# Performance work log

Hardware: AMD Instinct MI355X
Metric: run time of the kernel (lower is better)

The kernel has to match this reference:

```python
import jax, jax.numpy as jnp
import numpy as np

HISTORY = 128  # self-inclusive causal window width

def _layernorm(x, g, b, eps=1e-5):
    mu = jnp.mean(x, axis=-1, keepdims=True)
    var = jnp.var(x, axis=-1, keepdims=True)
    return (x - mu) * jax.lax.rsqrt(var + eps) * g + b

def setup_inputs() -> dict:
    key = jax.random.key(0)
    ks = jax.random.split(key, 8)
    dim, hid, B, T = 64, 256, 4, 4096
    s = lambda fan_in: 1.0 / np.sqrt(fan_in)
    return {
        "x": jax.random.normal(ks[0], (B, T, dim), jnp.float32),
        "W_in": jax.random.normal(ks[1], (dim, hid), jnp.float32) * s(dim),
        "b_in": jnp.zeros((hid,), jnp.float32),
        "W_qkv": jax.random.normal(ks[2], (hid, 3 * hid), jnp.float32) * s(hid),
        "b_qkv": jnp.zeros((3 * hid,), jnp.float32),
        "g_attn": jnp.ones((hid,), jnp.float32),
        "be_attn": jnp.zeros((hid,), jnp.float32),
        "g_mlp": jnp.ones((hid,), jnp.float32),
        "be_mlp": jnp.zeros((hid,), jnp.float32),
        "W1": jax.random.normal(ks[3], (hid, hid), jnp.float32) * s(hid),
        "b1": jnp.zeros((hid,), jnp.float32),
        "W2": jax.random.normal(ks[4], (hid, hid), jnp.float32) * s(hid),
        "b2": jnp.zeros((hid,), jnp.float32),
        "W_out": jax.random.normal(ks[5], (hid, dim), jnp.float32) * s(hid),
        "b_out": jnp.zeros((dim,), jnp.float32),
    }

def reference(x, W_in, b_in, W_qkv, b_qkv, g_attn, be_attn, g_mlp, be_mlp,
              W1, b1, W2, b2, W_out, b_out):
    B, T, _ = x.shape
    hid = W_in.shape[1]
    h = x @ W_in + b_in                                  # (B,T,hid)
    qkv = _layernorm(h, g_attn, be_attn) @ W_qkv + b_qkv
    q, k, v = jnp.split(qkv, 3, axis=-1)
    scale = 1.0 / jnp.sqrt(jnp.asarray(hid, x.dtype))
    scores = jnp.einsum('bqd,bkd->bqk', q, k) * scale    # (B,T,T)
    idx = jnp.arange(T)
    delta = idx[:, None] - idx[None, :]
    mask = (delta >= 0) & (delta <= HISTORY)             # self-inclusive window
    scores = jnp.where(mask[None], scores, jnp.finfo(x.dtype).min)
    attn = jax.nn.softmax(scores, axis=-1)
    attn_out = jnp.einsum('bqk,bkd->bqd', attn, v)
    h = h + attn_out                                     # residual (dropout=0)
    m = _layernorm(h, g_mlp, be_mlp)
    m = jax.nn.gelu(m @ W1 + b1, approximate=False) @ W2 + b2
    h = h + m
    return h @ W_out + b_out                             # (B,T,dim)
```

## Files before the change

kernel.cpp:

```cpp
#include <hip/hip_runtime.h>
#include <hip/hip_bf16.h>
#include <math.h>

typedef short bf8 __attribute__((ext_vector_type(8)));
typedef float f4  __attribute__((ext_vector_type(4)));

#define DEV static __device__ __forceinline__

DEV f4 MFMA(bf8 a, bf8 b, f4 c) { return __builtin_amdgcn_mfma_f32_16x16x32_bf16(a, b, c, 0, 0, 0); }

DEV unsigned short f2bf(float f) {
  union { float f; unsigned int u; } v; v.f = f;
  unsigned int r = v.u + 0x7FFFu + ((v.u >> 16) & 1u);
  return (unsigned short)(r >> 16);
}
DEV float bf2f(unsigned short u) {
  union { unsigned int u; float f; } v; v.u = ((unsigned int)u) << 16;
  return v.f;
}

struct P15 { const void* p[15]; };

DEV float ldin(const void* p, int i, bool bf) {
  return bf ? bf2f(((const unsigned short*)p)[i]) : ((const float*)p)[i];
}

#define PB_IN 0
#define PB_QKV 256
#define PB1 1024
#define PB2 1280
#define PB_OUT 1536
#define PGA 1600
#define PBA 1856
#define PGM 2112
#define PBM 2368

__global__ __launch_bounds__(256) void k_prep(P15 in,
    unsigned short* __restrict__ xb, unsigned short* __restrict__ WinT,
    unsigned short* __restrict__ WqkvT, unsigned short* __restrict__ W1T,
    unsigned short* __restrict__ W2T, unsigned short* __restrict__ WoutT,
    float* __restrict__ par)
{
  const bool bf = (*(const unsigned int*)in.p[5]) == 0x3F803F80u;
  const int E0 = 1048576;
  const int E1 = E0 + 16384;
  const int E2 = E1 + 196608;
  const int E3 = E2 + 65536;
  const int E4 = E3 + 65536;
  const int E5 = E4 + 16384;
  const int E6 = E5 + 2624;
  for (int i = blockIdx.x * 256 + threadIdx.x; i < E6; i += gridDim.x * 256) {
    if (i < E0) {
      xb[i] = f2bf(ldin(in.p[0], i, bf));
    } else if (i < E1) {
      int j = i - E0, n = j >> 6, k = j & 63;
      WinT[j] = f2bf(ldin(in.p[1], k * 256 + n, bf));
    } else if (i < E2) {
      int j = i - E1, n = j >> 8, k = j & 255;
      WqkvT[j] = f2bf(ldin(in.p[3], k * 768 + n, bf));
    } else if (i < E3) {
      int j = i - E2, n = j >> 8, k = j & 255;
      W1T[j] = f2bf(ldin(in.p[9], k * 256 + n, bf));
    } else if (i < E4) {
      int j = i - E3, n = j >> 8, k = j & 255;
      W2T[j] = f2bf(ldin(in.p[11], k * 256 + n, bf));
    } else if (i < E5) {
      int j = i - E4, n = j >> 8, k = j & 255;
      WoutT[j] = f2bf(ldin(in.p[13], k * 64 + n, bf));
    } else {
      int j = i - E5;
      const void* src; int o;
      if (j < 256)       { src = in.p[2];  o = j; }
      else if (j < 1024) { src = in.p[4];  o = j - 256; }
      else if (j < 1280) { src = in.p[10]; o = j - 1024; }
      else if (j < 1536) { src = in.p[12]; o = j - 1280; }
      else if (j < 1600) { src = in.p[14]; o = j - 1536; }
      else if (j < 1856) { src = in.p[5];  o = j - 1600; }
      else if (j < 2112) { src = in.p[6];  o = j - 1856; }
      else if (j < 2368) { src = in.p[7];  o = j - 2112; }
      else               { src = in.p[8];  o = j - 2368; }
      par[j] = ldin(src, o, bf);
    }
  }
}

__global__ __launch_bounds__(256) void k_in_ln(const unsigned short* __restrict__ xb,
    const unsigned short* __restrict__ WinT, const float* __restrict__ par,
    float* __restrict__ h, unsigned short* __restrict__ ln1)
{
  __shared__ unsigned short sA[64 * 72];
  __shared__ unsigned short sB[256 * 72];
  const int tid = threadIdx.x, lane = tid & 63, w = tid >> 6;
  const int l15 = lane & 15, l4 = lane >> 4;
  const int m0 = blockIdx.x * 64;
  for (int t = tid; t < 512; t += 256) {
    int r = t >> 3, c8 = (t & 7) * 8;
    *(bf8*)&sA[r * 72 + c8] = *(const bf8*)&xb[(m0 + r) * 64 + c8];
  }
  for (int t = tid; t < 2048; t += 256) {
    int r = t >> 3, c8 = (t & 7) * 8;
    *(bf8*)&sB[r * 72 + c8] = *(const bf8*)&WinT[r * 64 + c8];
  }
  __syncthreads();
  f4 z = {0.f, 0.f, 0.f, 0.f};
  f4 acc[16];
  #pragma unroll
  for (int f = 0; f < 16; ++f) acc[f] = z;
  #pragma unroll
  for (int ks = 0; ks < 2; ++ks) {
    bf8 a = *(const bf8*)&sA[(16 * w + l15) * 72 + ks * 32 + l4 * 8];
    #pragma unroll
    for (int f = 0; f < 16; ++f) {
      bf8 b = *(const bf8*)&sB[(16 * f + l15) * 72 + ks * 32 + l4 * 8];
      acc[f] = MFMA(a, b, acc[f]);
    }
  }
  float s[4] = {0,0,0,0}, s2[4] = {0,0,0,0};
  #pragma unroll
  for (int f = 0; f < 16; ++f) {
    float bias = par[PB_IN + 16 * f + l15];
    #pragma unroll
    for (int r = 0; r < 4; ++r) {
      float v = acc[f][r] + bias; acc[f][r] = v;
      s[r] += v; s2[r] += v * v;
    }
  }
  #pragma unroll
  for (int msk = 1; msk <= 8; msk <<= 1) {
    #pragma unroll
    for (int r = 0; r < 4; ++r) { s[r] += __shfl_xor(s[r], msk); s2[r] += __shfl_xor(s2[r], msk); }
  }
  float mu[4], rstd[4];
  #pragma unroll
  for (int r = 0; r < 4; ++r) {
    mu[r] = s[r] * (1.f / 256.f);
    float var = s2[r] * (1.f / 256.f) - mu[r] * mu[r];
    rstd[r] = rsqrtf(var + 1e-5f);
  }
  #pragma unroll
  for (int f = 0; f < 16; ++f) {
    int col = 16 * f + l15;
    float g = par[PGA + col], be = par[PBA + col];
    #pragma unroll
    for (int r = 0; r < 4; ++r) {
      int row = m0 + 16 * w + 4 * l4 + r;
      h[row * 256 + col] = acc[f][r];
      ln1[row * 256 + col] = f2bf((acc[f][r] - mu[r]) * rstd[r] * g + be);
    }
  }
}

__global__ __launch_bounds__(256) void k_qkv(const unsigned short* __restrict__ ln1,
    const unsigned short* __restrict__ WqkvT, const float* __restrict__ par,
    unsigned short* __restrict__ qb, unsigned short* __restrict__ kb,
    unsigned short* __restrict__ vT)
{
  __shared__ unsigned short sA[64 * 72];
  __shared__ unsigned short sB[64 * 72];
  const int tid = threadIdx.x, lane = tid & 63, w = tid >> 6;
  const int l15 = lane & 15, l4 = lane >> 4;
  const int mt = blockIdx.x / 12, nt = blockIdx.x % 12;
  const int m0 = mt * 64, n0 = nt * 64;
  const int wm = w >> 1, wn = w & 1;
  f4 z = {0.f, 0.f, 0.f, 0.f};
  f4 acc[2][2];
  acc[0][0] = z; acc[0][1] = z; acc[1][0] = z; acc[1][1] = z;
  for (int kc = 0; kc < 4; ++kc) {
    for (int t = tid; t < 512; t += 256) {
      int r = t >> 3, c8 = (t & 7) * 8;
      *(bf8*)&sA[r * 72 + c8] = *(const bf8*)&ln1[(m0 + r) * 256 + kc * 64 + c8];
    }
    for (int t = tid; t < 512; t += 256) {
      int r = t >> 3, c8 = (t & 7) * 8;
      *(bf8*)&sB[r * 72 + c8] = *(const bf8*)&WqkvT[(n0 + r) * 256 + kc * 64 + c8];
    }
    __syncthreads();
    #pragma unroll
    for (int ks = 0; ks < 2; ++ks) {
      bf8 a0 = *(const bf8*)&sA[(32 * wm + l15) * 72 + ks * 32 + l4 * 8];
      bf8 a1 = *(const bf8*)&sA[(32 * wm + 16 + l15) * 72 + ks * 32 + l4 * 8];
      bf8 b0 = *(const bf8*)&sB[(32 * wn + l15) * 72 + ks * 32 + l4 * 8];
      bf8 b1 = *(const bf8*)&sB[(32 * wn + 16 + l15) * 72 + ks * 32 + l4 * 8];
      acc[0][0] = MFMA(a0, b0, acc[0][0]);
      acc[0][1] = MFMA(a0, b1, acc[0][1]);
      acc[1][0] = MFMA(a1, b0, acc[1][0]);
      acc[1][1] = MFMA(a1, b1, acc[1][1]);
    }
    __syncthreads();
  }
  #pragma unroll
  for (int i = 0; i < 2; ++i) {
    #pragma unroll
    for (int j = 0; j < 2; ++j) {
      int col = n0 + 32 * wn + 16 * j + l15;
      float bias = par[PB_QKV + col];
      int seg = col >> 8, c = col & 255;
      #pragma unroll
      for (int r = 0; r < 4; ++r) {
        int row = m0 + 32 * wm + 16 * i + 4 * l4 + r;
        unsigned short ov = f2bf(acc[i][j][r] + bias);
        if (seg == 0) qb[row * 256 + c] = ov;
        else if (seg == 1) kb[row * 256 + c] = ov;
        else vT[((row >> 12) * 256 + c) * 4096 + (row & 4095)] = ov;
      }
    }
  }
}

__global__ __launch_bounds__(256) void k_attn(const unsigned short* __restrict__ qb,
    const unsigned short* __restrict__ kb, const unsigned short* __restrict__ vT,
    const float* __restrict__ h, const float* __restrict__ par,
    float* __restrict__ h2, unsigned short* __restrict__ ln2)
{
  __shared__ unsigned short sKV[256 * 72];
  __shared__ unsigned short sP[64 * 200];
  const int tid = threadIdx.x, lane = tid & 63, w = tid >> 6;
  const int l15 = lane & 15, l4 = lane >> 4;
  const int b = blockIdx.x >> 6, q0 = (blockIdx.x & 63) * 64;
  const int tok0 = b * 4096 + q0, kstart = q0 - 128;

  bf8 qreg[8];
  {
    const int qrow = tok0 + 16 * w + l15;
    #pragma unroll
    for (int ks = 0; ks < 8; ++ks)
      qreg[ks] = *(const bf8*)&qb[qrow * 256 + ks * 32 + l4 * 8];
  }

  f4 z = {0.f, 0.f, 0.f, 0.f};
  f4 sacc[12];
  #pragma unroll
  for (int i = 0; i < 12; ++i) sacc[i] = z;

  #pragma unroll
  for (int c = 0; c < 3; ++c) {
    for (int t = tid; t < 2048; t += 256) {
      int r = t >> 5, c8 = (t & 31) * 8;
      int j = kstart + 64 * c + r; if (j < 0) j = 0;
      *(bf8*)&sKV[r * 264 + c8] = *(const bf8*)&kb[(b * 4096 + j) * 256 + c8];
    }
    __syncthreads();
    #pragma unroll
    for (int ks = 0; ks < 8; ++ks) {
      #pragma unroll
      for (int fn = 0; fn < 4; ++fn) {
        bf8 bfr = *(const bf8*)&sKV[(16 * fn + l15) * 264 + ks * 32 + l4 * 8];
        sacc[4 * c + fn] = MFMA(qreg[ks], bfr, sacc[4 * c + fn]);
      }
    }
    __syncthreads();
  }

  const float scale = 0.0625f;
  float mx[4] = {-1e30f, -1e30f, -1e30f, -1e30f};
  #pragma unroll
  for (int c = 0; c < 3; ++c) {
    #pragma unroll
    for (int fn = 0; fn < 4; ++fn) {
      int kk = 64 * c + 16 * fn + l15;
      #pragma unroll
      for (int r = 0; r < 4; ++r) {
        int qi = 16 * w + 4 * l4 + r;
        bool valid = (kk >= qi) && (kk <= qi + 128) && (kstart + kk >= 0);
        float sv = valid ? sacc[4 * c + fn][r] * scale : -1e30f;
        sacc[4 * c + fn][r] = sv;
        mx[r] = fmaxf(mx[r], sv);
      }
    }
  }
  #pragma unroll
  for (int msk = 1; msk <= 8; msk <<= 1) {
    #pragma unroll
    for (int r = 0; r < 4; ++r) mx[r] = fmaxf(mx[r], __shfl_xor(mx[r], msk));
  }
  float sum[4] = {0,0,0,0};
  #pragma unroll
  for (int c = 0; c < 3; ++c) {
    #pragma unroll
    for (int fn = 0; fn < 4; ++fn) {
      #pragma unroll
      for (int r = 0; r < 4; ++r) {
        float p = __expf(sacc[4 * c + fn][r] - mx[r]);
        sacc[4 * c + fn][r] = p;
        sum[r] += p;
      }
    }
  }
  #pragma unroll
  for (int msk = 1; msk <= 8; msk <<= 1) {
    #pragma unroll
    for (int r = 0; r < 4; ++r) sum[r] += __shfl_xor(sum[r], msk);
  }
  #pragma unroll
  for (int c = 0; c < 3; ++c) {
    #pragma unroll
    for (int fn = 0; fn < 4; ++fn) {
      #pragma unroll
      for (int r = 0; r < 4; ++r) {
        int kk = 64 * c + 16 * fn + l15;
        sP[(16 * w + 4 * l4 + r) * 200 + kk] = f2bf(sacc[4 * c + fn][r]);
      }
    }
  }

  f4 oacc[16];
  #pragma unroll
  for (int f = 0; f < 16; ++f) oacc[f] = z;
  #pragma unroll
  for (int c = 0; c < 3; ++c) {
    for (int t = tid; t < 2048; t += 256) {
      int d = t >> 3, c8 = (t & 7) * 8;
      int j0 = kstart + 64 * c + c8; if (j0 < 0) j0 = 0;
      *(bf8*)&sKV[d * 72 + c8] = *(const bf8*)&vT[(b * 256 + d) * 4096 + j0];
    }
    __syncthreads();
    #pragma unroll
    for (int ks = 0; ks < 2; ++ks) {
      bf8 a = *(const bf8*)&sP[(16 * w + l15) * 200 + 64 * c + ks * 32 + l4 * 8];
      #pragma unroll
      for (int f = 0; f < 16; ++f) {
        bf8 bv = *(const bf8*)&sKV[(16 * f + l15) * 72 + ks * 32 + l4 * 8];
        oacc[f] = MFMA(a, bv, oacc[f]);
      }
    }
    __syncthreads();
  }

  float inv[4];
  #pragma unroll
  for (int r = 0; r < 4; ++r) inv[r] = 1.f / sum[r];
  float s[4] = {0,0,0,0}, s2[4] = {0,0,0,0};
  #pragma unroll
  for (int f = 0; f < 16; ++f) {
    int col = 16 * f + l15;
    #pragma unroll
    for (int r = 0; r < 4; ++r) {
      int row = tok0 + 16 * w + 4 * l4 + r;
      float v = h[row * 256 + col] + oacc[f][r] * inv[r];
      oacc[f][r] = v; s[r] += v; s2[r] += v * v;
    }
  }
  #pragma unroll
  for (int msk = 1; msk <= 8; msk <<= 1) {
    #pragma unroll
    for (int r = 0; r < 4; ++r) { s[r] += __shfl_xor(s[r], msk); s2[r] += __shfl_xor(s2[r], msk); }
  }
  float mu[4], rstd[4];
  #pragma unroll
  for (int r = 0; r < 4; ++r) {
    mu[r] = s[r] * (1.f / 256.f);
    float var = s2[r] * (1.f / 256.f) - mu[r] * mu[r];
    rstd[r] = rsqrtf(var + 1e-5f);
  }
  #pragma unroll
  for (int f = 0; f < 16; ++f) {
    int col = 16 * f + l15;
    float g = par[PGM + col], be = par[PBM + col];
    #pragma unroll
    for (int r = 0; r < 4; ++r) {
      int row = tok0 + 16 * w + 4 * l4 + r;
      h2[row * 256 + col] = oacc[f][r];
      ln2[row * 256 + col] = f2bf((oacc[f][r] - mu[r]) * rstd[r] * g + be);
    }
  }
}

__global__ __launch_bounds__(256) void k_mlp1(const unsigned short* __restrict__ ln2,
    const unsigned short* __restrict__ W1T, const float* __restrict__ par,
    unsigned short* __restrict__ m1)
{
  __shared__ unsigned short sA[64 * 72];
  __shared__ unsigned short sB[64 * 72];
  const int tid = threadIdx.x, lane = tid & 63, w = tid >> 6;
  const int l15 = lane & 15, l4 = lane >> 4;
  const int mt = blockIdx.x >> 2, nt = blockIdx.x & 3;
  const int m0 = mt * 64, n0 = nt * 64;
  const int wm = w >> 1, wn = w & 1;
  f4 z = {0.f, 0.f, 0.f, 0.f};
  f4 acc[2][2];
  acc[0][0] = z; acc[0][1] = z; acc[1][0] = z; acc[1][1] = z;
  for (int kc = 0; kc < 4; ++kc) {
    for (int t = tid; t < 512; t += 256) {
      int r = t >> 3, c8 = (t & 7) * 8;
      *(bf8*)&sA[r * 72 + c8] = *(const bf8*)&ln2[(m0 + r) * 256 + kc * 64 + c8];
    }
    for (int t = tid; t < 512; t += 256) {
      int r = t >> 3, c8 = (t & 7) * 8;
      *(bf8*)&sB[r * 72 + c8] = *(const bf8*)&W1T[(n0 + r) * 256 + kc * 64 + c8];
    }
    __syncthreads();
    #pragma unroll
    for (int ks = 0; ks < 2; ++ks) {
      bf8 a0 = *(const bf8*)&sA[(32 * wm + l15) * 72 + ks * 32 + l4 * 8];
      bf8 a1 = *(const bf8*)&sA[(32 * wm + 16 + l15) * 72 + ks * 32 + l4 * 8];
      bf8 b0 = *(const bf8*)&sB[(32 * wn + l15) * 72 + ks * 32 + l4 * 8];
      bf8 b1 = *(const bf8*)&sB[(32 * wn + 16 + l15) * 72 + ks * 32 + l4 * 8];
      acc[0][0] = MFMA(a0, b0, acc[0][0]);
      acc[0][1] = MFMA(a0, b1, acc[0][1]);
      acc[1][0] = MFMA(a1, b0, acc[1][0]);
      acc[1][1] = MFMA(a1, b1, acc[1][1]);
    }
    __syncthreads();
  }
  #pragma unroll
  for (int i = 0; i < 2; ++i) {
    #pragma unroll
    for (int j = 0; j < 2; ++j) {
      int col = n0 + 32 * wn + 16 * j + l15;
      float bias = par[PB1 + col];
      #pragma unroll
      for (int r = 0; r < 4; ++r) {
        int row = m0 + 32 * wm + 16 * i + 4 * l4 + r;
        float v = acc[i][j][r] + bias;
        float gl = 0.5f * v * (1.0f + erff(v * 0.70710678118654752f));
        m1[row * 256 + col] = f2bf(gl);
      }
    }
  }
}

__global__ __launch_bounds__(256) void k_mlp2_out(const unsigned short* __restrict__ m1,
    const unsigned short* __restrict__ W2T, const unsigned short* __restrict__ WoutT,
    const float* __restrict__ par, const float* __restrict__ h2,
    void* __restrict__ dout, const void* __restrict__ probe)
{
  __shared__ unsigned short sA[64 * 72];
  __shared__ unsigned short sB[256 * 72];
  __shared__ unsigned short sH[64 * 264];
  __shared__ unsigned short sW[64 * 264];
  const int tid = threadIdx.x, lane = tid & 63, w = tid >> 6;
  const int l15 = lane & 15, l4 = lane >> 4;
  const int m0 = blockIdx.x * 64;
  const bool obf = (*(const unsigned int*)probe) == 0x3F803F80u;

  for (int t = tid; t < 2048; t += 256) {
    int r = t >> 5, c8 = (t & 31) * 8;
    *(bf8*)&sW[r * 264 + c8] = *(const bf8*)&WoutT[r * 256 + c8];
  }
  f4 z = {0.f, 0.f, 0.f, 0.f};
  f4 acc[16];
  #pragma unroll
  for (int f = 0; f < 16; ++f) acc[f] = z;
  for (int kc = 0; kc < 4; ++kc) {
    for (int t = tid; t < 512; t += 256) {
      int r = t >> 3, c8 = (t & 7) * 8;
      *(bf8*)&sA[r * 72 + c8] = *(const bf8*)&m1[(m0 + r) * 256 + kc * 64 + c8];
    }
    for (int t = tid; t < 2048; t += 256) {
      int r = t >> 3, c8 = (t & 7) * 8;
      *(bf8*)&sB[r * 72 + c8] = *(const bf8*)&W2T[r * 256 + kc * 64 + c8];
    }
    __syncthreads();
    #pragma unroll
    for (int ks = 0; ks < 2; ++ks) {
      bf8 a = *(const bf8*)&sA[(16 * w + l15) * 72 + ks * 32 + l4 * 8];
      #pragma unroll
      for (int f = 0; f < 16; ++f) {
        bf8 b = *(const bf8*)&sB[(16 * f + l15) * 72 + ks * 32 + l4 * 8];
        acc[f] = MFMA(a, b, acc[f]);
      }
    }
    __syncthreads();
  }
  #pragma unroll
  for (int f = 0; f < 16; ++f) {
    int col = 16 * f + l15;
    float bias = par[PB2 + col];
    #pragma unroll
    for (int r = 0; r < 4; ++r) {
      int row_l = 16 * w + 4 * l4 + r;
      float v = h2[(m0 + row_l) * 256 + col] + acc[f][r] + bias;
      sH[row_l * 264 + col] = f2bf(v);
    }
  }
  f4 oacc[4];
  #pragma unroll
  for (int f = 0; f < 4; ++f) oacc[f] = z;
  #pragma unroll
  for (int ks = 0; ks < 8; ++ks) {
    bf8 a = *(const bf8*)&sH[(16 * w + l15) * 264 + ks * 32 + l4 * 8];
    #pragma unroll
    for (int fn = 0; fn < 4; ++fn) {
      bf8 bv = *(const bf8*)&sW[(16 * fn + l15) * 264 + ks * 32 + l4 * 8];
      oacc[fn] = MFMA(a, bv, oacc[fn]);
    }
  }
  #pragma unroll
  for (int fn = 0; fn < 4; ++fn) {
    int col = 16 * fn + l15;
    float bias = par[PB_OUT + col];
    #pragma unroll
    for (int r = 0; r < 4; ++r) {
      int row = m0 + 16 * w + 4 * l4 + r;
      float v = oacc[fn][r] + bias;
      if (obf) ((unsigned short*)dout)[row * 64 + col] = f2bf(v);
      else     ((float*)dout)[row * 64 + col] = v;
    }
  }
}

extern "C" void kernel_launch(void* const* d_in, const int* in_sizes, int n_in,
                              void* d_out, int out_size, void* d_ws, size_t ws_size,
                              hipStream_t stream)
{
  (void)in_sizes; (void)n_in; (void)out_size; (void)ws_size;
  char* ws = (char*)d_ws;
  size_t off = 0;
  auto A = [&](size_t bytes) { void* p = (void*)(ws + off); off += (bytes + 255) & ~(size_t)255; return p; };

  unsigned short* xb    = (unsigned short*)A(2097152);
  unsigned short* WinT  = (unsigned short*)A(32768);
  unsigned short* WqkvT = (unsigned short*)A(393216);
  unsigned short* W1T   = (unsigned short*)A(131072);
  unsigned short* W2T   = (unsigned short*)A(131072);
  unsigned short* WoutT = (unsigned short*)A(32768);
  float* par            = (float*)A(10496);
  float* h              = (float*)A(16777216);
  unsigned short* ln1   = (unsigned short*)A(8388608);
  unsigned short* qb    = (unsigned short*)A(8388608);
  unsigned short* kb    = (unsigned short*)A(8388608);
  unsigned short* vT    = (unsigned short*)A(8388608);
  float* h2             = (float*)A(16777216);
  unsigned short* ln2   = (unsigned short*)A(8388608);
  unsigned short* m1    = (unsigned short*)A(8388608);

  P15 in;
  for (int i = 0; i < 15; ++i) in.p[i] = d_in[i];

  k_prep    <<<dim3(1024), dim3(256), 0, stream>>>(in, xb, WinT, WqkvT, W1T, W2T, WoutT, par);
  k_in_ln   <<<dim3(256),  dim3(256), 0, stream>>>(xb, WinT, par, h, ln1);
  k_qkv     <<<dim3(3072), dim3(256), 0, stream>>>(ln1, WqkvT, par, qb, kb, vT);
  k_attn    <<<dim3(256),  dim3(256), 0, stream>>>(qb, kb, vT, h, par, h2, ln2);
  k_mlp1    <<<dim3(1024), dim3(256), 0, stream>>>(ln2, W1T, par, m1);
  k_mlp2_out<<<dim3(256),  dim3(256), 0, stream>>>(m1, W2T, WoutT, par, h2, d_out, d_in[5]);
}
```

Measured before the change: 180.2 us.

## Fuse input projection with QKV GEMM and MLP1 with MLP2/output projection

Merges the input-projection+LayerNorm kernel with the QKV GEMM, and the two MLP GEMMs with the output projection, into single 512-thread kernels. Intermediates (ln1, m1) stay in LDS instead of round-tripping through global memory, and the fp32-to-bf16 conversion of x moves from the prep kernel into the fused kernel. Launch count drops from six to four. In exchange each fused kernel runs only 256 blocks, reads B weights straight from global or L2 without LDS staging, and carries heavy register and LDS use, which may lower occupancy.

```diff
diff --git a/kernel.cpp b/kernel.cpp
--- a/kernel.cpp
+++ b/kernel.cpp
@@ -36,39 +36,35 @@
 #define PBM 2368
 
 __global__ __launch_bounds__(256) void k_prep(P15 in,
-    unsigned short* __restrict__ xb, unsigned short* __restrict__ WinT,
-    unsigned short* __restrict__ WqkvT, unsigned short* __restrict__ W1T,
-    unsigned short* __restrict__ W2T, unsigned short* __restrict__ WoutT,
-    float* __restrict__ par)
+    unsigned short* __restrict__ WinT, unsigned short* __restrict__ WqkvT,
+    unsigned short* __restrict__ W1T, unsigned short* __restrict__ W2T,
+    unsigned short* __restrict__ WoutT, float* __restrict__ par)
 {
   const bool bf = (*(const unsigned int*)in.p[5]) == 0x3F803F80u;
-  const int E0 = 1048576;
-  const int E1 = E0 + 16384;
-  const int E2 = E1 + 196608;
+  const int E0 = 16384;
+  const int E1 = E0 + 196608;
+  const int E2 = E1 + 65536;
   const int E3 = E2 + 65536;
-  const int E4 = E3 + 65536;
-  const int E5 = E4 + 16384;
-  const int E6 = E5 + 2624;
-  for (int i = blockIdx.x * 256 + threadIdx.x; i < E6; i += gridDim.x * 256) {
+  const int E4 = E3 + 16384;
+  const int E5 = E4 + 2624;
+  for (int i = blockIdx.x * 256 + threadIdx.x; i < E5; i += gridDim.x * 256) {
     if (i < E0) {
-      xb[i] = f2bf(ldin(in.p[0], i, bf));
+      int n = i >> 6, k = i & 63;
+      WinT[i] = f2bf(ldin(in.p[1], k * 256 + n, bf));
     } else if (i < E1) {
-      int j = i - E0, n = j >> 6, k = j & 63;
-      WinT[j] = f2bf(ldin(in.p[1], k * 256 + n, bf));
+      int j = i - E0, n = j >> 8, k = j & 255;
+      WqkvT[j] = f2bf(ldin(in.p[3], k * 768 + n, bf));
     } else if (i < E2) {
       int j = i - E1, n = j >> 8, k = j & 255;
-      WqkvT[j] = f2bf(ldin(in.p[3], k * 768 + n, bf));
+      W1T[j] = f2bf(ldin(in.p[9], k * 256 + n, bf));
     } else if (i < E3) {
       int j = i - E2, n = j >> 8, k = j & 255;
-      W1T[j] = f2bf(ldin(in.p[9], k * 256 + n, bf));
+      W2T[j] = f2bf(ldin(in.p[11], k * 256 + n, bf));
     } else if (i < E4) {
       int j = i - E3, n = j >> 8, k = j & 255;
-      W2T[j] = f2bf(ldin(in.p[11], k * 256 + n, bf));
-    } else if (i < E5) {
-      int j = i - E4, n = j >> 8, k = j & 255;
       WoutT[j] = f2bf(ldin(in.p[13], k * 64 + n, bf));
     } else {
-      int j = i - E5;
+      int j = i - E4;
       const void* src; int o;
       if (j < 256)       { src = in.p[2];  o = j; }
       else if (j < 1024) { src = in.p[4];  o = j - 256; }
@@ -84,126 +80,146 @@
   }
 }
 
-__global__ __launch_bounds__(256) void k_in_ln(const unsigned short* __restrict__ xb,
-    const unsigned short* __restrict__ WinT, const float* __restrict__ par,
-    float* __restrict__ h, unsigned short* __restrict__ ln1)
+__global__ __launch_bounds__(512, 2) void k_in_qkv(const void* __restrict__ xin,
+    const unsigned short* __restrict__ WinT, const unsigned short* __restrict__ WqkvT,
+    const float* __restrict__ par, const void* __restrict__ probe,
+    float* __restrict__ h, unsigned short* __restrict__ qb,
+    unsigned short* __restrict__ kb, unsigned short* __restrict__ vT)
 {
-  __shared__ unsigned short sA[64 * 72];
-  __shared__ unsigned short sB[256 * 72];
+  __shared__ unsigned short smem[33280 + 18432];
+  __shared__ float sStat[8][16][2];
+  unsigned short* sQK = smem;
+  unsigned short* sX  = smem;
+  unsigned short* sW  = smem + 4608;
+  unsigned short* sLn = smem + 33280;
+  unsigned short* sV  = smem + 33280;
   const int tid = threadIdx.x, lane = tid & 63, w = tid >> 6;
   const int l15 = lane & 15, l4 = lane >> 4;
   const int m0 = blockIdx.x * 64;
-  for (int t = tid; t < 512; t += 256) {
+  const bool bf = (*(const unsigned int*)probe) == 0x3F803F80u;
+
+  {
+    int r = tid >> 3, c8 = (tid & 7) * 8;
+    if (bf) {
+      *(bf8*)&sX[r * 72 + c8] = *(const bf8*)((const unsigned short*)xin + (m0 + r) * 64 + c8);
+    } else {
+      const float* xf = (const float*)xin + (m0 + r) * 64 + c8;
+      float4 f0 = *(const float4*)xf, f1 = *(const float4*)(xf + 4);
+      unsigned short t8[8] = { f2bf(f0.x), f2bf(f0.y), f2bf(f0.z), f2bf(f0.w),
+                               f2bf(f1.x), f2bf(f1.y), f2bf(f1.z), f2bf(f1.w) };
+      *(bf8*)&sX[r * 72 + c8] = *(const bf8*)t8;
+    }
+  }
+  for (int t = tid; t < 2048; t += 512) {
     int r = t >> 3, c8 = (t & 7) * 8;
-    *(bf8*)&sA[r * 72 + c8] = *(const bf8*)&xb[(m0 + r) * 64 + c8];
-  }
-  for (int t = tid; t < 2048; t += 256) {
-    int r = t >> 3, c8 = (t & 7) * 8;
-    *(bf8*)&sB[r * 72 + c8] = *(const bf8*)&WinT[r * 64 + c8];
-  }
-  __syncthreads();
+    *(bf8*)&sW[r * 72 + c8] = *(const bf8*)&WinT[r * 64 + c8];
+  }
+  __syncthreads();
+
+  const int rm = w & 3, cg = w >> 2;
   f4 z = {0.f, 0.f, 0.f, 0.f};
-  f4 acc[16];
-  #pragma unroll
-  for (int f = 0; f < 16; ++f) acc[f] = z;
-  #pragma unroll
-  for (int ks = 0; ks < 2; ++ks) {
-    bf8 a = *(const bf8*)&sA[(16 * w + l15) * 72 + ks * 32 + l4 * 8];
-    #pragma unroll
-    for (int f = 0; f < 16; ++f) {
-      bf8 b = *(const bf8*)&sB[(16 * f + l15) * 72 + ks * 32 + l4 * 8];
-      acc[f] = MFMA(a, b, acc[f]);
-    }
+  f4 acc1[8];
+  #pragma unroll
+  for (int f = 0; f < 8; ++f) acc1[f] = z;
+  bf8 ax0 = *(const bf8*)&sX[(16 * rm + l15) * 72 + l4 * 8];
+  bf8 ax1 = *(const bf8*)&sX[(16 * rm + l15) * 72 + 32 + l4 * 8];
+  #pragma unroll
+  for (int f = 0; f < 8; ++f) {
+    bf8 b0 = *(const bf8*)&sW[(128 * cg + 16 * f + l15) * 72 + l4 * 8];
+    bf8 b1 = *(const bf8*)&sW[(128 * cg + 16 * f + l15) * 72 + 32 + l4 * 8];
+    acc1[f] = MFMA(ax0, b0, acc1[f]);
+    acc1[f] = MFMA(ax1, b1, acc1[f]);
   }
   float s[4] = {0,0,0,0}, s2[4] = {0,0,0,0};
   #pragma unroll
-  for (int f = 0; f < 16; ++f) {
-    float bias = par[PB_IN + 16 * f + l15];
+  for (int f = 0; f < 8; ++f) {
+    float bias = par[PB_IN + 128 * cg + 16 * f + l15];
     #pragma unroll
     for (int r = 0; r < 4; ++r) {
-      float v = acc[f][r] + bias; acc[f][r] = v;
+      float v = acc1[f][r] + bias; acc1[f][r] = v;
       s[r] += v; s2[r] += v * v;
     }
   }
   #pragma unroll
-  for (int msk = 1; msk <= 8; msk <<= 1) {
-    #pragma unroll
-    for (int r = 0; r < 4; ++r) { s[r] += __shfl_xor(s[r], msk); s2[r] += __shfl_xor(s2[r], msk); }
-  }
+  for (int m = 1; m <= 8; m <<= 1) {
+    #pragma unroll
+    for (int r = 0; r < 4; ++r) { s[r] += __shfl_xor(s[r], m); s2[r] += __shfl_xor(s2[r], m); }
+  }
+  if (l15 == 0) {
+    #pragma unroll
+    for (int r = 0; r < 4; ++r) { sStat[w][4 * l4 + r][0] = s[r]; sStat[w][4 * l4 + r][1] = s2[r]; }
+  }
+  __syncthreads();
   float mu[4], rstd[4];
   #pragma unroll
   for (int r = 0; r < 4; ++r) {
-    mu[r] = s[r] * (1.f / 256.f);
-    float var = s2[r] * (1.f / 256.f) - mu[r] * mu[r];
-    rstd[r] = rsqrtf(var + 1e-5f);
-  }
-  #pragma unroll
-  for (int f = 0; f < 16; ++f) {
-    int col = 16 * f + l15;
+    float st  = s[r]  + sStat[w ^ 4][4 * l4 + r][0];
+    float st2 = s2[r] + sStat[w ^ 4][4 * l4 + r][1];
+    mu[r] = st * (1.f / 256.f);
+    rstd[r] = rsqrtf(st2 * (1.f / 256.f) - mu[r] * mu[r] + 1e-5f);
+  }
+  #pragma unroll
+  for (int f = 0; f < 8; ++f) {
+    int col = 128 * cg + 16 * f + l15;
     float g = par[PGA + col], be = par[PBA + col];
     #pragma unroll
     for (int r = 0; r < 4; ++r) {
-      int row = m0 + 16 * w + 4 * l4 + r;
-      h[row * 256 + col] = acc[f][r];
-      ln1[row * 256 + col] = f2bf((acc[f][r] - mu[r]) * rstd[r] * g + be);
-    }
-  }
-}
-
-__global__ __launch_bounds__(256) void k_qkv(const unsigned short* __restrict__ ln1,
-    const unsigned short* __restrict__ WqkvT, const float* __restrict__ par,
-    unsigned short* __restrict__ qb, unsigned short* __restrict__ kb,
-    unsigned short* __restrict__ vT)
-{
-  __shared__ unsigned short sA[64 * 72];
-  __shared__ unsigned short sB[64 * 72];
-  const int tid = threadIdx.x, lane = tid & 63, w = tid >> 6;
-  const int l15 = lane & 15, l4 = lane >> 4;
-  const int mt = blockIdx.x / 12, nt = blockIdx.x % 12;
-  const int m0 = mt * 64, n0 = nt * 64;
-  const int wm = w >> 1, wn = w & 1;
-  f4 z = {0.f, 0.f, 0.f, 0.f};
-  f4 acc[2][2];
-  acc[0][0] = z; acc[0][1] = z; acc[1][0] = z; acc[1][1] = z;
-  for (int kc = 0; kc < 4; ++kc) {
-    for (int t = tid; t < 512; t += 256) {
-      int r = t >> 3, c8 = (t & 7) * 8;
-      *(bf8*)&sA[r * 72 + c8] = *(const bf8*)&ln1[(m0 + r) * 256 + kc * 64 + c8];
-    }
-    for (int t = tid; t < 512; t += 256) {
-      int r = t >> 3, c8 = (t & 7) * 8;
-      *(bf8*)&sB[r * 72 + c8] = *(const bf8*)&WqkvT[(n0 + r) * 256 + kc * 64 + c8];
-    }
-    __syncthreads();
-    #pragma unroll
-    for (int ks = 0; ks < 2; ++ks) {
-      bf8 a0 = *(const bf8*)&sA[(32 * wm + l15) * 72 + ks * 32 + l4 * 8];
-      bf8 a1 = *(const bf8*)&sA[(32 * wm + 16 + l15) * 72 + ks * 32 + l4 * 8];
-      bf8 b0 = *(const bf8*)&sB[(32 * wn + l15) * 72 + ks * 32 + l4 * 8];
-      bf8 b1 = *(const bf8*)&sB[(32 * wn + 16 + l15) * 72 + ks * 32 + l4 * 8];
-      acc[0][0] = MFMA(a0, b0, acc[0][0]);
-      acc[0][1] = MFMA(a0, b1, acc[0][1]);
-      acc[1][0] = MFMA(a1, b0, acc[1][0]);
-      acc[1][1] = MFMA(a1, b1, acc[1][1]);
-    }
-    __syncthreads();
+      int rl = 16 * rm + 4 * l4 + r;
+      h[(m0 + rl) * 256 + col] = acc1[f][r];
+      sLn[rl * 264 + col] = f2bf((acc1[f][r] - mu[r]) * rstd[r] * g + be);
+    }
+  }
+  __syncthreads();
+
+  const int rm2 = w & 1, cg2 = w >> 1;
+  bf8 a2[2][8];
+  #pragma unroll
+  for (int i = 0; i < 2; ++i)
+    #pragma unroll
+    for (int ks = 0; ks < 8; ++ks)
+      a2[i][ks] = *(const bf8*)&sLn[(32 * rm2 + 16 * i + l15) * 264 + ks * 32 + l4 * 8];
+  __syncthreads();
+  f4 acc2[2][12];
+  #pragma unroll
+  for (int i = 0; i < 2; ++i)
+    #pragma unroll
+    for (int f = 0; f < 12; ++f) acc2[i][f] = z;
+  #pragma unroll
+  for (int f = 0; f < 12; ++f) {
+    const unsigned short* bp = &WqkvT[(192 * cg2 + 16 * f + l15) * 256 + l4 * 8];
+    #pragma unroll
+    for (int ks = 0; ks < 8; ++ks) {
+      bf8 b = *(const bf8*)&bp[ks * 32];
+      acc2[0][f] = MFMA(a2[0][ks], b, acc2[0][f]);
+      acc2[1][f] = MFMA(a2[1][ks], b, acc2[1][f]);
+    }
   }
   #pragma unroll
   for (int i = 0; i < 2; ++i) {
     #pragma unroll
-    for (int j = 0; j < 2; ++j) {
-      int col = n0 + 32 * wn + 16 * j + l15;
+    for (int f = 0; f < 12; ++f) {
+      int col = 192 * cg2 + 16 * f + l15;
       float bias = par[PB_QKV + col];
-      int seg = col >> 8, c = col & 255;
+      int rl = 32 * rm2 + 16 * i + 4 * l4;
       #pragma unroll
       for (int r = 0; r < 4; ++r) {
-        int row = m0 + 32 * wm + 16 * i + 4 * l4 + r;
-        unsigned short ov = f2bf(acc[i][j][r] + bias);
-        if (seg == 0) qb[row * 256 + c] = ov;
-        else if (seg == 1) kb[row * 256 + c] = ov;
-        else vT[((row >> 12) * 256 + c) * 4096 + (row & 4095)] = ov;
-      }
-    }
+        unsigned short bv = f2bf(acc2[i][f][r] + bias);
+        if (col < 512) sQK[(rl + r) * 520 + col] = bv;
+        else           sV[(col - 512) * 72 + rl + r] = bv;
+      }
+    }
+  }
+  __syncthreads();
+  const int bb = m0 >> 12, t0 = m0 & 4095;
+  for (int ch = tid; ch < 4096; ch += 512) {
+    int r = ch >> 6, c8 = (ch & 63) * 8;
+    bf8 v = *(const bf8*)&sQK[r * 520 + c8];
+    if (c8 < 256) *(bf8*)&qb[(m0 + r) * 256 + c8] = v;
+    else          *(bf8*)&kb[(m0 + r) * 256 + (c8 - 256)] = v;
+  }
+  for (int ch = tid; ch < 2048; ch += 512) {
+    int d = ch >> 3, c8 = (ch & 7) * 8;
+    *(bf8*)&vT[(bb * 256 + d) * 4096 + t0 + c8] = *(const bf8*)&sV[d * 72 + c8];
   }
 }
 
@@ -365,136 +381,132 @@
   }
 }
 
-__global__ __launch_bounds__(256) void k_mlp1(const unsigned short* __restrict__ ln2,
-    const unsigned short* __restrict__ W1T, const float* __restrict__ par,
-    unsigned short* __restrict__ m1)
+__global__ __launch_bounds__(512, 2) void k_mlp_out(const unsigned short* __restrict__ ln2,
+    const unsigned short* __restrict__ W1T, const unsigned short* __restrict__ W2T,
+    const unsigned short* __restrict__ WoutT, const float* __restrict__ par,
+    const float* __restrict__ h2, void* __restrict__ dout, const void* __restrict__ probe)
 {
-  __shared__ unsigned short sA[64 * 72];
-  __shared__ unsigned short sB[64 * 72];
-  const int tid = threadIdx.x, lane = tid & 63, w = tid >> 6;
-  const int l15 = lane & 15, l4 = lane >> 4;
-  const int mt = blockIdx.x >> 2, nt = blockIdx.x & 3;
-  const int m0 = mt * 64, n0 = nt * 64;
-  const int wm = w >> 1, wn = w & 1;
-  f4 z = {0.f, 0.f, 0.f, 0.f};
-  f4 acc[2][2];
-  acc[0][0] = z; acc[0][1] = z; acc[1][0] = z; acc[1][1] = z;
-  for (int kc = 0; kc < 4; ++kc) {
-    for (int t = tid; t < 512; t += 256) {
-      int r = t >> 3, c8 = (t & 7) * 8;
-      *(bf8*)&sA[r * 72 + c8] = *(const bf8*)&ln2[(m0 + r) * 256 + kc * 64 + c8];
-    }
-    for (int t = tid; t < 512; t += 256) {
-      int r = t >> 3, c8 = (t & 7) * 8;
-      *(bf8*)&sB[r * 72 + c8] = *(const bf8*)&W1T[(n0 + r) * 256 + kc * 64 + c8];
-    }
-    __syncthreads();
-    #pragma unroll
-    for (int ks = 0; ks < 2; ++ks) {
-      bf8 a0 = *(const bf8*)&sA[(32 * wm + l15) * 72 + ks * 32 + l4 * 8];
-      bf8 a1 = *(const bf8*)&sA[(32 * wm + 16 + l15) * 72 + ks * 32 + l4 * 8];
-      bf8 b0 = *(const bf8*)&sB[(32 * wn + l15) * 72 + ks * 32 + l4 * 8];
-      bf8 b1 = *(const bf8*)&sB[(32 * wn + 16 + l15) * 72 + ks * 32 + l4 * 8];
-      acc[0][0] = MFMA(a0, b0, acc[0][0]);
-      acc[0][1] = MFMA(a0, b1, acc[0][1]);
-      acc[1][0] = MFMA(a1, b0, acc[1][0]);
-      acc[1][1] = MFMA(a1, b1, acc[1][1]);
-    }
-    __syncthreads();
-  }
-  #pragma unroll
-  for (int i = 0; i < 2; ++i) {
-    #pragma unroll
-    for (int j = 0; j < 2; ++j) {
-      int col = n0 + 32 * wn + 16 * j + l15;
-      float bias = par[PB1 + col];
-      #pragma unroll
-      for (int r = 0; r < 4; ++r) {
-        int row = m0 + 32 * wm + 16 * i + 4 * l4 + r;
-        float v = acc[i][j][r] + bias;
-        float gl = 0.5f * v * (1.0f + erff(v * 0.70710678118654752f));
-        m1[row * 256 + col] = f2bf(gl);
-      }
-    }
-  }
-}
-
-__global__ __launch_bounds__(256) void k_mlp2_out(const unsigned short* __restrict__ m1,
-    const unsigned short* __restrict__ W2T, const unsigned short* __restrict__ WoutT,
-    const float* __restrict__ par, const float* __restrict__ h2,
-    void* __restrict__ dout, const void* __restrict__ probe)
-{
-  __shared__ unsigned short sA[64 * 72];
-  __shared__ unsigned short sB[256 * 72];
+  __shared__ unsigned short sL[64 * 264];
+  __shared__ unsigned short sM[64 * 264];
   __shared__ unsigned short sH[64 * 264];
-  __shared__ unsigned short sW[64 * 264];
   const int tid = threadIdx.x, lane = tid & 63, w = tid >> 6;
   const int l15 = lane & 15, l4 = lane >> 4;
   const int m0 = blockIdx.x * 64;
   const bool obf = (*(const unsigned int*)probe) == 0x3F803F80u;
 
-  for (int t = tid; t < 2048; t += 256) {
+  for (int t = tid; t < 2048; t += 512) {
     int r = t >> 5, c8 = (t & 31) * 8;
-    *(bf8*)&sW[r * 264 + c8] = *(const bf8*)&WoutT[r * 256 + c8];
-  }
+    *(bf8*)&sL[r * 264 + c8] = *(const bf8*)&ln2[(m0 + r) * 256 + c8];
+  }
+  __syncthreads();
+  const int rm2 = w & 1, cg = w >> 1;
   f4 z = {0.f, 0.f, 0.f, 0.f};
-  f4 acc[16];
-  #pragma unroll
-  for (int f = 0; f < 16; ++f) acc[f] = z;
-  for (int kc = 0; kc < 4; ++kc) {
-    for (int t = tid; t < 512; t += 256) {
-      int r = t >> 3, c8 = (t & 7) * 8;
-      *(bf8*)&sA[r * 72 + c8] = *(const bf8*)&m1[(m0 + r) * 256 + kc * 64 + c8];
-    }
-    for (int t = tid; t < 2048; t += 256) {
-      int r = t >> 3, c8 = (t & 7) * 8;
-      *(bf8*)&sB[r * 72 + c8] = *(const bf8*)&W2T[r * 256 + kc * 64 + c8];
-    }
-    __syncthreads();
-    #pragma unroll
-    for (int ks = 0; ks < 2; ++ks) {
-      bf8 a = *(const bf8*)&sA[(16 * w + l15) * 72 + ks * 32 + l4 * 8];
-      #pragma unroll
-      for (int f = 0; f < 16; ++f) {
-        bf8 b = *(const bf8*)&sB[(16 * f + l15) * 72 + ks * 32 + l4 * 8];
-        acc[f] = MFMA(a, b, acc[f]);
-      }
-    }
-    __syncthreads();
-  }
-  #pragma unroll
-  for (int f = 0; f < 16; ++f) {
-    int col = 16 * f + l15;
-    float bias = par[PB2 + col];
-    #pragma unroll
-    for (int r = 0; r < 4; ++r) {
-      int row_l = 16 * w + 4 * l4 + r;
-      float v = h2[(m0 + row_l) * 256 + col] + acc[f][r] + bias;
-      sH[row_l * 264 + col] = f2bf(v);
-    }
-  }
-  f4 oacc[4];
-  #pragma unroll
-  for (int f = 0; f < 4; ++f) oacc[f] = z;
-  #pragma unroll
-  for (int ks = 0; ks < 8; ++ks) {
-    bf8 a = *(const bf8*)&sH[(16 * w + l15) * 264 + ks * 32 + l4 * 8];
-    #pragma unroll
-    for (int fn = 0; fn < 4; ++fn) {
-      bf8 bv = *(const bf8*)&sW[(16 * fn + l15) * 264 + ks * 32 + l4 * 8];
-      oacc[fn] = MFMA(a, bv, oacc[fn]);
-    }
-  }
-  #pragma unroll
-  for (int fn = 0; fn < 4; ++fn) {
-    int col = 16 * fn + l15;
+
+  {
+    bf8 a[2][8];
+    #pragma unroll
+    for (int i = 0; i < 2; ++i)
+      #pragma unroll
+      for (int ks = 0; ks < 8; ++ks)
+        a[i][ks] = *(const bf8*)&sL[(32 * rm2 + 16 * i + l15) * 264 + ks * 32 + l4 * 8];
+    f4 acc[2][4];
+    #pragma unroll
+    for (int i = 0; i < 2; ++i)
+      #pragma unroll
+      for (int f = 0; f < 4; ++f) acc[i][f] = z;
+    #pragma unroll
+    for (int f = 0; f < 4; ++f) {
+      const unsigned short* bp = &W1T[(64 * cg + 16 * f + l15) * 256 + l4 * 8];
+      #pragma unroll
+      for (int ks = 0; ks < 8; ++ks) {
+        bf8 b = *(const bf8*)&bp[ks * 32];
+        acc[0][f] = MFMA(a[0][ks], b, acc[0][f]);
+        acc[1][f] = MFMA(a[1][ks], b, acc[1][f]);
+      }
+    }
+    #pragma unroll
+    for (int i = 0; i < 2; ++i) {
+      #pragma unroll
+      for (int f = 0; f < 4; ++f) {
+        int col = 64 * cg + 16 * f + l15;
+        float bias = par[PB1 + col];
+        #pragma unroll
+        for (int r = 0; r < 4; ++r) {
+          float v = acc[i][f][r] + bias;
+          float gl = 0.5f * v * (1.0f + erff(v * 0.70710678118654752f));
+          sM[(32 * rm2 + 16 * i + 4 * l4 + r) * 264 + col] = f2bf(gl);
+        }
+      }
+    }
+  }
+  __syncthreads();
+
+  {
+    bf8 a[2][8];
+    #pragma unroll
+    for (int i = 0; i < 2; ++i)
+      #pragma unroll
+      for (int ks = 0; ks < 8; ++ks)
+        a[i][ks] = *(const bf8*)&sM[(32 * rm2 + 16 * i + l15) * 264 + ks * 32 + l4 * 8];
+    f4 acc[2][4];
+    #pragma unroll
+    for (int i = 0; i < 2; ++i)
+      #pragma unroll
+      for (int f = 0; f < 4; ++f) acc[i][f] = z;
+    #pragma unroll
+    for (int f = 0; f < 4; ++f) {
+      const unsigned short* bp = &W2T[(64 * cg + 16 * f + l15) * 256 + l4 * 8];
+      #pragma unroll
+      for (int ks = 0; ks < 8; ++ks) {
+        bf8 b = *(const bf8*)&bp[ks * 32];
+        acc[0][f] = MFMA(a[0][ks], b, acc[0][f]);
+        acc[1][f] = MFMA(a[1][ks], b, acc[1][f]);
+      }
+    }
+    #pragma unroll
+    for (int i = 0; i < 2; ++i) {
+      #pragma unroll
+      for (int f = 0; f < 4; ++f) {
+        int col = 64 * cg + 16 * f + l15;
+        float bias = par[PB2 + col];
+        #pragma unroll
+        for (int r = 0; r < 4; ++r) {
+          int row = 32 * rm2 + 16 * i + 4 * l4 + r;
+          float v = h2[(m0 + row) * 256 + col] + acc[i][f][r] + bias;
+          sH[row * 264 + col] = f2bf(v);
+        }
+      }
+    }
+  }
+  __syncthreads();
+
+  {
+    bf8 a[2][8];
+    #pragma unroll
+    for (int i = 0; i < 2; ++i)
+      #pragma unroll
+      for (int ks = 0; ks < 8; ++ks)
+        a[i][ks] = *(const bf8*)&sH[(32 * rm2 + 16 * i + l15) * 264 + ks * 32 + l4 * 8];
+    f4 acc[2];
+    acc[0] = z; acc[1] = z;
+    const unsigned short* bp = &WoutT[(16 * cg + l15) * 256 + l4 * 8];
+    #pragma unroll
+    for (int ks = 0; ks < 8; ++ks) {
+      bf8 b = *(const bf8*)&bp[ks * 32];
+      acc[0] = MFMA(a[0][ks], b, acc[0]);
+      acc[1] = MFMA(a[1][ks], b, acc[1]);
+    }
+    int col = 16 * cg + l15;
     float bias = par[PB_OUT + col];
     #pragma unroll
-    for (int r = 0; r < 4; ++r) {
-      int row = m0 + 16 * w + 4 * l4 + r;
-      float v = oacc[fn][r] + bias;
-      if (obf) ((unsigned short*)dout)[row * 64 + col] = f2bf(v);
-      else     ((float*)dout)[row * 64 + col] = v;
+    for (int i = 0; i < 2; ++i) {
+      #pragma unroll
+      for (int r = 0; r < 4; ++r) {
+        int row = m0 + 32 * rm2 + 16 * i + 4 * l4 + r;
+        float v = acc[i][r] + bias;
+        if (obf) ((unsigned short*)dout)[row * 64 + col] = f2bf(v);
+        else     ((float*)dout)[row * 64 + col] = v;
+      }
     }
   }
 }
@@ -508,7 +520,6 @@
   size_t off = 0;
   auto A = [&](size_t bytes) { void* p = (void*)(ws + off); off += (bytes + 255) & ~(size_t)255; return p; };
 
-  unsigned short* xb    = (unsigned short*)A(2097152);
   unsigned short* WinT  = (unsigned short*)A(32768);
   unsigned short* WqkvT = (unsigned short*)A(393216);
   unsigned short* W1T   = (unsigned short*)A(131072);
@@ -516,21 +527,17 @@
   unsigned short* WoutT = (unsigned short*)A(32768);
   float* par            = (float*)A(10496);
   float* h              = (float*)A(16777216);
-  unsigned short* ln1   = (unsigned short*)A(8388608);
   unsigned short* qb    = (unsigned short*)A(8388608);
   unsigned short* kb    = (unsigned short*)A(8388608);
   unsigned short* vT    = (unsigned short*)A(8388608);
   float* h2             = (float*)A(16777216);
   unsigned short* ln2   = (unsigned short*)A(8388608);
-  unsigned short* m1    = (unsigned short*)A(8388608);
 
   P15 in;
   for (int i = 0; i < 15; ++i) in.p[i] = d_in[i];
 
-  k_prep    <<<dim3(1024), dim3(256), 0, stream>>>(in, xb, WinT, WqkvT, W1T, W2T, WoutT, par);
-  k_in_ln   <<<dim3(256),  dim3(256), 0, stream>>>(xb, WinT, par, h, ln1);
-  k_qkv     <<<dim3(3072), dim3(256), 0, stream>>>(ln1, WqkvT, par, qb, kb, vT);
-  k_attn    <<<dim3(256),  dim3(256), 0, stream>>>(qb, kb, vT, h, par, h2, ln2);
-  k_mlp1    <<<dim3(1024), dim3(256), 0, stream>>>(ln2, W1T, par, m1);
-  k_mlp2_out<<<dim3(256),  dim3(256), 0, stream>>>(m1, W2T, WoutT, par, h2, d_out, d_in[5]);
-}
+  k_prep   <<<dim3(1419), dim3(256), 0, stream>>>(in, WinT, WqkvT, W1T, W2T, WoutT, par);
+  k_in_qkv <<<dim3(256),  dim3(512), 0, stream>>>(d_in[0], WinT, WqkvT, par, d_in[5], h, qb, kb, vT);
+  k_attn   <<<dim3(256),  dim3(256), 0, stream>>>(qb, kb, vT, h, par, h2, ln2);
+  k_mlp_out<<<dim3(256),  dim3(512), 0, stream>>>(ln2, W1T, W2T, WoutT, par, h2, d_out, d_in[5]);
+}
```

Result: faster. 175.7 us (-2.5%).
